# Kernel optimization log

Hardware: AMD Instinct MI355X
Metric: run time of the kernel (lower is better)

The kernel has to match this reference:

```python
import jax, jax.numpy as jnp
import numpy as np

NUM_HEADS = 4


def setup_inputs() -> dict:
    key = jax.random.key(0)
    ks = jax.random.split(key, 12)
    N, E_edges, ND, ED, D, G = 50000, 800000, 128, 64, 256, 128
    h = jax.random.normal(ks[0], (N, ND), dtype=jnp.float32)
    edge_index = jax.random.randint(ks[1], (2, E_edges), 0, N)
    edge_attr = jax.random.normal(ks[2], (E_edges, ED), dtype=jnp.float32)
    batch = jnp.sort(jax.random.randint(ks[3], (N,), 0, G))
    node_w = jax.random.normal(ks[4], (D, ND), dtype=jnp.float32) / np.sqrt(ND)
    node_b = jnp.zeros((D,), dtype=jnp.float32)
    edge_w = jax.random.normal(ks[5], (D, ED), dtype=jnp.float32) / np.sqrt(ED)
    edge_b = jnp.zeros((D,), dtype=jnp.float32)
    query = jax.random.normal(ks[6], (1, D), dtype=jnp.float32)
    in_w = jax.random.normal(ks[7], (3 * D, D), dtype=jnp.float32) / np.sqrt(D)
    in_b = jnp.zeros((3 * D,), dtype=jnp.float32)
    out_w = jax.random.normal(ks[8], (D, D), dtype=jnp.float32) / np.sqrt(D)
    out_b = jnp.zeros((D,), dtype=jnp.float32)
    return {"h": h, "edge_index": edge_index, "edge_attr": edge_attr, "batch": batch,
            "num_graphs": G, "node_w": node_w, "node_b": node_b,
            "edge_w": edge_w, "edge_b": edge_b, "query": query,
            "in_w": in_w, "in_b": in_b, "out_w": out_w, "out_b": out_b}


def reference(h, edge_index, edge_attr, batch, num_graphs,
              node_w, node_b, edge_w, edge_b, query, in_w, in_b, out_w, out_b):
    N = h.shape[0]
    D = query.shape[-1]
    dh = D // NUM_HEADS
    G = num_graphs
    # node projection
    h_proj = h @ node_w.T + node_b  # [N, D]
    # scatter-mean edge features to source nodes
    row = edge_index[0]
    e_proj = edge_attr @ edge_w.T + edge_b  # [E, D]
    e_sum = jax.ops.segment_sum(e_proj, row, num_segments=N)
    cnt = jax.ops.segment_sum(jnp.ones((row.shape[0],), jnp.float32), row, num_segments=N)
    h_proj = h_proj + e_sum / jnp.maximum(cnt, 1.0)[:, None]
    # per-graph single-query multi-head attention (torch MultiheadAttention math)
    wq, wk, wv = in_w[:D], in_w[D:2 * D], in_w[2 * D:]
    bq, bk, bv = in_b[:D], in_b[D:2 * D], in_b[2 * D:]
    q = (query @ wq.T + bq).reshape(NUM_HEADS, dh)            # [H, dh]
    k = (h_proj @ wk.T + bk).reshape(N, NUM_HEADS, dh)        # [N, H, dh]
    v = (h_proj @ wv.T + bv).reshape(N, NUM_HEADS, dh)        # [N, H, dh]
    scores = jnp.einsum('hd,nhd->nh', q, k) / jnp.sqrt(jnp.float32(dh))  # [N, H]
    smax = jax.ops.segment_max(scores, batch, num_segments=G)  # [G, H]
    w = jnp.exp(scores - smax[batch])                          # [N, H]
    denom = jax.ops.segment_sum(w, batch, num_segments=G)      # [G, H]
    p = w / jnp.maximum(denom[batch], 1e-30)                   # [N, H]
    pooled = jax.ops.segment_sum(p[:, :, None] * v, batch, num_segments=G)  # [G, H, dh]
    out = pooled.reshape(G, 1, D) @ out_w.T + out_b            # [G, 1, D]
    return out
```

## Files before the change

### kernel.cpp

```cpp
#include <hip/hip_runtime.h>
#include <hip/hip_bf16.h>
#include <math.h>

#define NDIM 128
#define EDIM 64
#define DDIM 256
#define NSPLIT 4
#define CAP 96
#define SNODES 32

typedef __attribute__((ext_vector_type(8))) short short8;

__device__ inline ushort f2bf(float x) {
    uint32_t u = __float_as_uint(x);
    uint32_t r = (u + 0x7fff + ((u >> 16) & 1)) >> 16;
    return (ushort)r;
}
__device__ inline float bf2f(ushort h) { return __uint_as_float(((uint32_t)h) << 16); }

__global__ __launch_bounds__(256) void k_setup(
    int* __restrict__ zero_p, int n_zero, int ZBLK,
    const float* __restrict__ node_w, const float* __restrict__ edge_w,
    const float* __restrict__ node_b, const float* __restrict__ edge_b,
    const float* __restrict__ query, const float* __restrict__ in_w,
    const float* __restrict__ in_b, float* __restrict__ prep)
{
    const int tid = threadIdx.x;
    int b = blockIdx.x;
    if (b < ZBLK) {
        int i = b * 256 + tid;
        if (i < n_zero) zero_p[i] = 0;
        return;
    }
    __shared__ float q_s[DDIM];
    __shared__ float qv[DDIM];
    __shared__ float qk_s[4 * DDIM];
    __shared__ float sb_s[4];
    q_s[tid] = query[tid];
    __syncthreads();
    float acc = in_b[tid];
    const float* wq = in_w + (size_t)tid * DDIM;
    for (int i = 0; i < DDIM; ++i) acc += q_s[i] * wq[i];
    qv[tid] = acc;
    __syncthreads();
    for (int h = 0; h < 4; ++h) {
        float a = 0.f;
        for (int d = 0; d < 64; ++d)
            a += qv[h * 64 + d] * in_w[(size_t)(DDIM + h * 64 + d) * DDIM + tid];
        qk_s[h * DDIM + tid] = a;
    }
    if (tid < 4) {
        float a = 0.f;
        for (int d = 0; d < 64; ++d) a += qv[tid * 64 + d] * in_b[DDIM + tid * 64 + d];
        sb_s[tid] = a;
    }
    __syncthreads();
    for (int idx = tid; idx < 4 * NDIM; idx += 256) {
        int hh = idx >> 7, k = idx & 127;
        float a = 0.f;
        for (int j = 0; j < DDIM; ++j) a += qk_s[hh * DDIM + j] * node_w[(size_t)j * NDIM + k];
        prep[idx] = a;
    }
    {
        int hh = tid >> 6, k = tid & 63;
        float a = 0.f;
        for (int j = 0; j < DDIM; ++j) a += qk_s[hh * DDIM + j] * edge_w[(size_t)j * EDIM + k];
        prep[4 * NDIM + tid] = a;
    }
    if (tid < 4) {
        float a = 0.f, e = 0.f;
        for (int j = 0; j < DDIM; ++j) {
            a += node_b[j] * qk_s[tid * DDIM + j];
            e += edge_b[j] * qk_s[tid * DDIM + j];
        }
        prep[4 * NDIM + 256 + tid] = a + sb_s[tid];
        prep[4 * NDIM + 260 + tid] = e;
    }
}

__global__ __launch_bounds__(256) void k_scatbin(
    const int* __restrict__ erow, const float* __restrict__ edge_attr,
    int* __restrict__ fill, ushort* __restrict__ ebin, int E)
{
    int gid = blockIdx.x * 256 + threadIdx.x;
    int e = gid >> 3;
    int seg8 = gid & 7;
    if (e >= E) return;
    int r = erow[e];
    int pos = 0;
    if (seg8 == 0) pos = atomicAdd(&fill[r], 1);
    pos = __shfl(pos, 0, 8);
    if (pos >= CAP) return;
    const float* ea = edge_attr + (size_t)e * EDIM + seg8 * 8;
    float4 va = *reinterpret_cast<const float4*>(ea);
    float4 vb = *reinterpret_cast<const float4*>(ea + 4);
    short8 o;
    o[0] = (short)f2bf(va.x); o[1] = (short)f2bf(va.y);
    o[2] = (short)f2bf(va.z); o[3] = (short)f2bf(va.w);
    o[4] = (short)f2bf(vb.x); o[5] = (short)f2bf(vb.y);
    o[6] = (short)f2bf(vb.z); o[7] = (short)f2bf(vb.w);
    *reinterpret_cast<short8*>(
        ebin + ((size_t)r * CAP + pos) * EDIM + seg8 * 8) = o;
}

__global__ __launch_bounds__(256) void k_score(
    const float* __restrict__ h, const ushort* __restrict__ ebin,
    const int* __restrict__ fill, const float* __restrict__ prep,
    ushort* __restrict__ agg_bf, float* __restrict__ scores, int N)
{
    __shared__ float qkn_s[4 * NDIM];
    __shared__ float qke_s[4 * EDIM];
    __shared__ float cst[8];
    const int tid = threadIdx.x;
    for (int i = tid; i < 4 * NDIM; i += 256) qkn_s[i] = prep[i];
    qke_s[tid] = prep[4 * NDIM + tid];
    if (tid < 8) cst[tid] = prep[4 * NDIM + 256 + tid];
    __syncthreads();

    const int node = blockIdx.x * SNODES + (tid >> 3);
    const int seg8 = tid & 7;
    if (node >= N) return;
    const int cnt = fill[node];
    const float inv = 1.f / fmaxf((float)cnt, 1.f);
    const float fl = (cnt > 0) ? 1.f : 0.f;

    float hd[4] = {0.f, 0.f, 0.f, 0.f};
    const float4* hp = reinterpret_cast<const float4*>(h + (size_t)node * NDIM + seg8 * 16);
#pragma unroll
    for (int q = 0; q < 4; ++q) {
        float4 hv = hp[q];
        int base = seg8 * 16 + q * 4;
#pragma unroll
        for (int hh = 0; hh < 4; ++hh) {
            const float* qp = &qkn_s[hh * NDIM + base];
            hd[hh] += hv.x * qp[0] + hv.y * qp[1] + hv.z * qp[2] + hv.w * qp[3];
        }
    }

    float a[8];
#pragma unroll
    for (int i = 0; i < 8; ++i) a[i] = 0.f;
    {
        const ushort* eb = ebin + (size_t)node * CAP * EDIM + seg8 * 8;
        int c = min(cnt, CAP);
        int j = 0;
        for (; j + 3 < c; j += 4) {
            short8 v0 = *reinterpret_cast<const short8*>(eb + (size_t)(j + 0) * EDIM);
            short8 v1 = *reinterpret_cast<const short8*>(eb + (size_t)(j + 1) * EDIM);
            short8 v2 = *reinterpret_cast<const short8*>(eb + (size_t)(j + 2) * EDIM);
            short8 v3 = *reinterpret_cast<const short8*>(eb + (size_t)(j + 3) * EDIM);
#pragma unroll
            for (int i = 0; i < 8; ++i)
                a[i] += (bf2f((ushort)v0[i]) + bf2f((ushort)v1[i]))
                      + (bf2f((ushort)v2[i]) + bf2f((ushort)v3[i]));
        }
        for (; j < c; ++j) {
            short8 v0 = *reinterpret_cast<const short8*>(eb + (size_t)j * EDIM);
#pragma unroll
            for (int i = 0; i < 8; ++i) a[i] += bf2f((ushort)v0[i]);
        }
    }
    {
        short8 o;
#pragma unroll
        for (int i = 0; i < 8; ++i) o[i] = (short)f2bf(a[i]);
        *reinterpret_cast<short8*>(agg_bf + (size_t)node * EDIM + seg8 * 8) = o;
    }
    float ed[4] = {0.f, 0.f, 0.f, 0.f};
#pragma unroll
    for (int i = 0; i < 8; ++i) {
#pragma unroll
        for (int hh = 0; hh < 4; ++hh)
            ed[hh] += a[i] * qke_s[hh * EDIM + seg8 * 8 + i];
    }
    float t[4];
#pragma unroll
    for (int hh = 0; hh < 4; ++hh) t[hh] = hd[hh] + ed[hh] * inv;
#pragma unroll
    for (int off = 1; off < 8; off <<= 1) {
#pragma unroll
        for (int hh = 0; hh < 4; ++hh) t[hh] += __shfl_xor(t[hh], off);
    }
    if (seg8 == 0) {
        float4 sc;
        sc.x = (t[0] + cst[0] + fl * cst[4]) * 0.125f;
        sc.y = (t[1] + cst[1] + fl * cst[5]) * 0.125f;
        sc.z = (t[2] + cst[2] + fl * cst[6]) * 0.125f;
        sc.w = (t[3] + cst[3] + fl * cst[7]) * 0.125f;
        *reinterpret_cast<float4*>(scores + (size_t)node * 4) = sc;
    }
}

__global__ __launch_bounds__(256) void k_pool(
    const float* __restrict__ h, const ushort* __restrict__ agg_bf,
    const float* __restrict__ scores, const int* __restrict__ batch,
    const int* __restrict__ fill,
    float* __restrict__ pm, float* __restrict__ pdn, float* __restrict__ pe,
    float* __restrict__ pv, float* __restrict__ pu, int N)
{
    __shared__ float sc_s[256 * 4];
    __shared__ float cn_s[256];
    __shared__ float red_a[16];
    __shared__ float red_b[16];
    __shared__ float vred[2][4][NDIM];
    __shared__ float ured[4][4][EDIM];

    const int b = blockIdx.x;
    const int g = b >> 2;
    const int part = b & 3;
    const int tid = threadIdx.x;
    const int lane = tid & 63;
    const int wave = tid >> 6;
    const int dv = tid & 127;
    const int g2 = tid >> 7;
    const int du = tid & 63;
    const int g4 = tid >> 6;

    int lo = 0, hi = N;
    while (lo < hi) { int mid = (lo + hi) >> 1; if (batch[mid] < g) lo = mid + 1; else hi = mid; }
    const int s = lo;
    hi = N;
    while (lo < hi) { int mid = (lo + hi) >> 1; if (batch[mid] < g + 1) lo = mid + 1; else hi = mid; }
    const int e = lo;
    const int len = e - s;
    const int cs = s + (len * part) / NSPLIT;
    const int ce = s + (len * (part + 1)) / NSPLIT;

    float m[4], dn[4], spe[4], v[4], uh[4];
#pragma unroll
    for (int hh = 0; hh < 4; ++hh) {
        m[hh] = -INFINITY; dn[hh] = 0.f; spe[hh] = 0.f; v[hh] = 0.f; uh[hh] = 0.f;
    }

    const int hsel = tid & 3;

    for (int c = cs; c < ce; c += 256) {
        int cn = min(256, ce - c);
        __syncthreads();
        if (tid < cn) {
            *reinterpret_cast<float4*>(&sc_s[tid * 4]) =
                *reinterpret_cast<const float4*>(scores + (size_t)(c + tid) * 4);
            cn_s[tid] = (float)fill[c + tid];
        }
        __syncthreads();

        float lm = -INFINITY;
        for (int n = tid >> 2; n < cn; n += 64) lm = fmaxf(lm, sc_s[n * 4 + hsel]);
#pragma unroll
        for (int off = 4; off < 64; off <<= 1) lm = fmaxf(lm, __shfl_xor(lm, off));
        if (lane < 4) red_a[wave * 4 + lane] = lm;
        __syncthreads();

        float nm[4];
#pragma unroll
        for (int hh = 0; hh < 4; ++hh) {
            float cm = fmaxf(fmaxf(red_a[hh], red_a[4 + hh]),
                             fmaxf(red_a[8 + hh], red_a[12 + hh]));
            nm[hh] = fmaxf(m[hh], cm);
            float sc = expf(m[hh] - nm[hh]);
            dn[hh] *= sc; spe[hh] *= sc; v[hh] *= sc; uh[hh] *= sc;
            m[hh] = nm[hh];
        }
        __syncthreads();

        float mh = (hsel == 0) ? nm[0] : (hsel == 1) ? nm[1] : (hsel == 2) ? nm[2] : nm[3];
        float ld = 0.f, le = 0.f;
        for (int idx = tid; idx < cn * 4; idx += 256) {
            float wv = expf(sc_s[idx] - mh);
            sc_s[idx] = wv;
            ld += wv;
            le += wv * ((cn_s[idx >> 2] > 0.5f) ? 1.f : 0.f);
        }
#pragma unroll
        for (int off = 4; off < 64; off <<= 1) {
            ld += __shfl_xor(ld, off);
            le += __shfl_xor(le, off);
        }
        if (lane < 4) { red_a[wave * 4 + lane] = ld; red_b[wave * 4 + lane] = le; }
        __syncthreads();
#pragma unroll
        for (int hh = 0; hh < 4; ++hh) {
            dn[hh]  += red_a[hh] + red_a[4 + hh] + red_a[8 + hh] + red_a[12 + hh];
            spe[hh] += red_b[hh] + red_b[4 + hh] + red_b[8 + hh] + red_b[12 + hh];
        }

        for (int ln = g2; ln < cn; ln += 2) {
            float val = h[(size_t)(c + ln) * NDIM + dv];
            float4 w4 = *reinterpret_cast<const float4*>(&sc_s[ln * 4]);
            v[0] += w4.x * val; v[1] += w4.y * val;
            v[2] += w4.z * val; v[3] += w4.w * val;
        }
        for (int ln = g4; ln < cn; ln += 4) {
            float val = bf2f(agg_bf[(size_t)(c + ln) * EDIM + du]);
            float ci = 1.f / fmaxf(cn_s[ln], 1.f);
            float4 w4 = *reinterpret_cast<const float4*>(&sc_s[ln * 4]);
            uh[0] += w4.x * ci * val; uh[1] += w4.y * ci * val;
            uh[2] += w4.z * ci * val; uh[3] += w4.w * ci * val;
        }
    }

    __syncthreads();
#pragma unroll
    for (int hh = 0; hh < 4; ++hh) {
        vred[g2][hh][dv] = v[hh];
        ured[g4][hh][du] = uh[hh];
    }
    __syncthreads();

    if (tid < 4) { pm[b * 4 + tid] = m[tid]; pdn[b * 4 + tid] = dn[tid]; pe[b * 4 + tid] = spe[tid]; }
    for (int idx = tid; idx < 4 * NDIM; idx += 256) {
        int hh = idx >> 7, k = idx & 127;
        pv[(size_t)(b * 4 + hh) * NDIM + k] = vred[0][hh][k] + vred[1][hh][k];
    }
    {
        int hh = tid >> 6, k = tid & 63;
        pu[(size_t)(b * 4 + hh) * EDIM + k] =
            ured[0][hh][k] + ured[1][hh][k] + ured[2][hh][k] + ured[3][hh][k];
    }
}

__global__ __launch_bounds__(256) void k_out(
    const float* __restrict__ pm, const float* __restrict__ pdn, const float* __restrict__ pe,
    const float* __restrict__ pv, const float* __restrict__ pu,
    const float* __restrict__ node_w, const float* __restrict__ edge_w,
    const float* __restrict__ node_b, const float* __restrict__ edge_b,
    const float* __restrict__ in_w, const float* __restrict__ in_b,
    const float* __restrict__ out_w, const float* __restrict__ out_b,
    float* __restrict__ out)
{
    __shared__ float vm[4][NDIM];
    __shared__ float um[4][EDIM];
    __shared__ float scp_s[NSPLIT][4];
    __shared__ float dnm_s[4];
    __shared__ float spe_s[4];
    __shared__ float has_s;
    __shared__ float hb_s[4 * DDIM];
    __shared__ float po_s[DDIM];

    const int g = blockIdx.x;
    const int tid = threadIdx.x;
    const int b0 = NSPLIT * g;

    if (tid < 4) {
        float Mh = -INFINITY;
#pragma unroll
        for (int p = 0; p < NSPLIT; ++p) Mh = fmaxf(Mh, pm[(b0 + p) * 4 + tid]);
        float d = 0.f, ee = 0.f;
#pragma unroll
        for (int p = 0; p < NSPLIT; ++p) {
            float mp = pm[(b0 + p) * 4 + tid];
            float scp = (mp == -INFINITY) ? 0.f : expf(mp - Mh);
            scp_s[p][tid] = scp;
            d += pdn[(b0 + p) * 4 + tid] * scp;
            ee += pe[(b0 + p) * 4 + tid] * scp;
        }
        dnm_s[tid] = d;
        spe_s[tid] = ee;
        if (tid == 0) has_s = (Mh > -INFINITY) ? 1.f : 0.f;
    }
    __syncthreads();

    for (int idx = tid; idx < 4 * NDIM; idx += 256) {
        int hh = idx >> 7, k = idx & 127;
        float a = 0.f;
#pragma unroll
        for (int p = 0; p < NSPLIT; ++p)
            a += pv[(size_t)((b0 + p) * 4 + hh) * NDIM + k] * scp_s[p][hh];
        vm[hh][k] = a;
    }
    {
        int hh = tid >> 6, k = tid & 63;
        float a = 0.f;
#pragma unroll
        for (int p = 0; p < NSPLIT; ++p)
            a += pu[(size_t)((b0 + p) * 4 + hh) * EDIM + k] * scp_s[p][hh];
        um[hh][k] = a;
    }
    __syncthreads();

    {
        int j = tid;
        float acch[4];
        float nbj = node_b[j], ebj = edge_b[j];
#pragma unroll
        for (int hh = 0; hh < 4; ++hh) acch[hh] = dnm_s[hh] * nbj + spe_s[hh] * ebj;
        const float4* nwr = reinterpret_cast<const float4*>(node_w + (size_t)j * NDIM);
        for (int q = 0; q < NDIM / 4; ++q) {
            float4 w4 = nwr[q];
#pragma unroll
            for (int hh = 0; hh < 4; ++hh) {
                const float* vp = &vm[hh][q * 4];
                acch[hh] += w4.x * vp[0] + w4.y * vp[1] + w4.z * vp[2] + w4.w * vp[3];
            }
        }
        const float4* ewr = reinterpret_cast<const float4*>(edge_w + (size_t)j * EDIM);
        for (int q = 0; q < EDIM / 4; ++q) {
            float4 w4 = ewr[q];
#pragma unroll
            for (int hh = 0; hh < 4; ++hh) {
                const float* up = &um[hh][q * 4];
                acch[hh] += w4.x * up[0] + w4.y * up[1] + w4.z * up[2] + w4.w * up[3];
            }
        }
#pragma unroll
        for (int hh = 0; hh < 4; ++hh)
            hb_s[hh * DDIM + j] = acch[hh] / fmaxf(dnm_s[hh], 1e-30f);
    }
    __syncthreads();

    const int jh = tid >> 6;
    const float* wv_row = in_w + (size_t)(2 * DDIM + tid) * DDIM;
    const float* hbr = &hb_s[jh * DDIM];
    float p = 0.f;
    for (int i = 0; i < DDIM; i += 4) {
        float4 a = *reinterpret_cast<const float4*>(hbr + i);
        float4 bb = *reinterpret_cast<const float4*>(wv_row + i);
        p += a.x * bb.x + a.y * bb.y + a.z * bb.z + a.w * bb.w;
    }
    p = (p + in_b[2 * DDIM + tid]) * has_s;
    po_s[tid] = p;
    __syncthreads();

    const float* ow_row = out_w + (size_t)tid * DDIM;
    float o = out_b[tid];
    for (int i = 0; i < DDIM; i += 4) {
        float4 a = *reinterpret_cast<const float4*>(&po_s[i]);
        float4 bb = *reinterpret_cast<const float4*>(ow_row + i);
        o += a.x * bb.x + a.y * bb.y + a.z * bb.z + a.w * bb.w;
    }
    out[(size_t)g * DDIM + tid] = o;
}

extern "C" void kernel_launch(void* const* d_in, const int* in_sizes, int n_in,
                              void* d_out, int out_size, void* d_ws, size_t ws_size,
                              hipStream_t stream) {
    const float* h         = (const float*)d_in[0];
    const int*   edge_idx  = (const int*)d_in[1];
    const float* edge_attr = (const float*)d_in[2];
    const int*   batch     = (const int*)d_in[3];
    const float* node_w    = (const float*)d_in[5];
    const float* node_b    = (const float*)d_in[6];
    const float* edge_w    = (const float*)d_in[7];
    const float* edge_b    = (const float*)d_in[8];
    const float* query     = (const float*)d_in[9];
    const float* in_w      = (const float*)d_in[10];
    const float* in_b      = (const float*)d_in[11];
    const float* out_w     = (const float*)d_in[12];
    const float* out_b     = (const float*)d_in[13];
    float* out = (float*)d_out;

    const int N = in_sizes[0] / NDIM;
    const int E = in_sizes[2] / EDIM;
    const int G = out_size / DDIM;

    char* ws = (char*)d_ws;
    size_t off = 0;
    auto alloc = [&](size_t bytes) { void* p = ws + off; off += (bytes + 255) & ~(size_t)255; return p; };

    int*    fill    = (int*)alloc((size_t)N * 4);
    float*  scores  = (float*)alloc((size_t)N * 4 * 4);
    ushort* agg_bf  = (ushort*)alloc((size_t)N * EDIM * 2);
    float*  prep    = (float*)alloc(776 * 4);
    float*  pm      = (float*)alloc((size_t)NSPLIT * G * 4 * 4);
    float*  pdn     = (float*)alloc((size_t)NSPLIT * G * 4 * 4);
    float*  pe      = (float*)alloc((size_t)NSPLIT * G * 4 * 4);
    float*  pv      = (float*)alloc((size_t)NSPLIT * G * 4 * NDIM * 4);
    float*  pu      = (float*)alloc((size_t)NSPLIT * G * 4 * EDIM * 4);
    ushort* ebin    = (ushort*)alloc((size_t)N * CAP * EDIM * 2);

    const int ZBLK = (N + 255) / 256;
    k_setup<<<ZBLK + 1, 256, 0, stream>>>(
        fill, N, ZBLK, node_w, edge_w, node_b, edge_b, query, in_w, in_b, prep);

    k_scatbin<<<((E * 8) + 255) / 256, 256, 0, stream>>>(
        edge_idx, edge_attr, fill, ebin, E);

    k_score<<<(N + SNODES - 1) / SNODES, 256, 0, stream>>>(
        h, ebin, fill, prep, agg_bf, scores, N);

    k_pool<<<NSPLIT * G, 256, 0, stream>>>(
        h, agg_bf, scores, batch, fill, pm, pdn, pe, pv, pu, N);

    k_out<<<G, 256, 0, stream>>>(
        pm, pdn, pe, pv, pu, node_w, edge_w, node_b, edge_b,
        in_w, in_b, out_w, out_b, out);
}
```

Baseline: 196.9 us.

## Replace fixed-capacity edge bins with exact CSR layout via histogram and prefix scan

Edges were previously binned per source node into fixed slots of capacity 96, and edges beyond that capacity were dropped. The change builds a histogram of source rows, runs a two-pass prefix scan to get per-node offsets, and scatters bf16 edge features into a compact CSR buffer sized by the edge count. This shrinks the bin buffer and makes the per-node edge reads contiguous. It also removes the silent truncation, so results stay correct for any degree. In exchange it adds three small kernel launches and a second pass over the edge indices. k_scan3 sums the block totals with one 64-lane wavefront, so it assumes N is at most 64*1024.

```diff
diff --git a/kernel.cpp b/kernel.cpp
--- a/kernel.cpp
+++ b/kernel.cpp
@@ -6,7 +6,6 @@
 #define EDIM 64
 #define DDIM 256
 #define NSPLIT 4
-#define CAP 96
 #define SNODES 32
 
 typedef __attribute__((ext_vector_type(8))) short short8;
@@ -78,9 +77,73 @@
     }
 }
 
+__global__ __launch_bounds__(256) void k_hist(
+    const int* __restrict__ erow, int* __restrict__ cnt, int E)
+{
+    int e = blockIdx.x * 256 + threadIdx.x;
+    if (e < E) atomicAdd(&cnt[erow[e]], 1);
+}
+
+__global__ __launch_bounds__(256) void k_scan1(
+    const int* __restrict__ cnt, int* __restrict__ blocksum, int N)
+{
+    int tid = threadIdx.x;
+    int i0 = blockIdx.x * 1024 + tid * 4;
+    int s = 0;
+#pragma unroll
+    for (int k = 0; k < 4; ++k) { int i = i0 + k; if (i < N) s += cnt[i]; }
+#pragma unroll
+    for (int off = 1; off < 64; off <<= 1) s += __shfl_xor(s, off);
+    __shared__ int ws4[4];
+    if ((tid & 63) == 0) ws4[tid >> 6] = s;
+    __syncthreads();
+    if (tid == 0) blocksum[blockIdx.x] = ws4[0] + ws4[1] + ws4[2] + ws4[3];
+}
+
+__global__ __launch_bounds__(256) void k_scan3(
+    const int* __restrict__ cnt, const int* __restrict__ blocksum,
+    int* __restrict__ base, int N)
+{
+    const int tid = threadIdx.x;
+    const int lane = tid & 63;
+    const int wv = tid >> 6;
+    const int b = blockIdx.x;
+    const int i0 = b * 1024 + tid * 4;
+
+    int v[4];
+#pragma unroll
+    for (int k = 0; k < 4; ++k) { int i = i0 + k; v[k] = (i < N) ? cnt[i] : 0; }
+    int tsum = v[0] + v[1] + v[2] + v[3];
+
+    int incl = tsum;
+#pragma unroll
+    for (int off = 1; off < 64; off <<= 1) {
+        int x = __shfl_up(incl, off);
+        if (lane >= off) incl += x;
+    }
+    __shared__ int wsum[4];
+    if (lane == 63) wsum[wv] = incl;
+    __syncthreads();
+    int wpre = 0;
+    for (int w = 0; w < wv; ++w) wpre += wsum[w];
+
+    int bb = (lane < b) ? blocksum[lane] : 0;
+#pragma unroll
+    for (int off = 1; off < 64; off <<= 1) bb += __shfl_xor(bb, off);
+
+    int excl = bb + wpre + incl - tsum;
+#pragma unroll
+    for (int k = 0; k < 4; ++k) {
+        int i = i0 + k;
+        if (i < N) base[i] = excl;
+        excl += v[k];
+    }
+}
+
 __global__ __launch_bounds__(256) void k_scatbin(
     const int* __restrict__ erow, const float* __restrict__ edge_attr,
-    int* __restrict__ fill, ushort* __restrict__ ebin, int E)
+    const int* __restrict__ base, int* __restrict__ fill,
+    ushort* __restrict__ ebin, int E)
 {
     int gid = blockIdx.x * 256 + threadIdx.x;
     int e = gid >> 3;
@@ -88,9 +151,8 @@
     if (e >= E) return;
     int r = erow[e];
     int pos = 0;
-    if (seg8 == 0) pos = atomicAdd(&fill[r], 1);
+    if (seg8 == 0) pos = base[r] + atomicAdd(&fill[r], 1);
     pos = __shfl(pos, 0, 8);
-    if (pos >= CAP) return;
     const float* ea = edge_attr + (size_t)e * EDIM + seg8 * 8;
     float4 va = *reinterpret_cast<const float4*>(ea);
     float4 vb = *reinterpret_cast<const float4*>(ea + 4);
@@ -99,13 +161,13 @@
     o[2] = (short)f2bf(va.z); o[3] = (short)f2bf(va.w);
     o[4] = (short)f2bf(vb.x); o[5] = (short)f2bf(vb.y);
     o[6] = (short)f2bf(vb.z); o[7] = (short)f2bf(vb.w);
-    *reinterpret_cast<short8*>(
-        ebin + ((size_t)r * CAP + pos) * EDIM + seg8 * 8) = o;
+    *reinterpret_cast<short8*>(ebin + (size_t)pos * EDIM + seg8 * 8) = o;
 }
 
 __global__ __launch_bounds__(256) void k_score(
     const float* __restrict__ h, const ushort* __restrict__ ebin,
-    const int* __restrict__ fill, const float* __restrict__ prep,
+    const int* __restrict__ base, const int* __restrict__ cnt,
+    const float* __restrict__ prep,
     ushort* __restrict__ agg_bf, float* __restrict__ scores, int N)
 {
     __shared__ float qkn_s[4 * NDIM];
@@ -120,19 +182,20 @@
     const int node = blockIdx.x * SNODES + (tid >> 3);
     const int seg8 = tid & 7;
     if (node >= N) return;
-    const int cnt = fill[node];
-    const float inv = 1.f / fmaxf((float)cnt, 1.f);
-    const float fl = (cnt > 0) ? 1.f : 0.f;
+    const int c = cnt[node];
+    const int bs = base[node];
+    const float inv = 1.f / fmaxf((float)c, 1.f);
+    const float fl = (c > 0) ? 1.f : 0.f;
 
     float hd[4] = {0.f, 0.f, 0.f, 0.f};
     const float4* hp = reinterpret_cast<const float4*>(h + (size_t)node * NDIM + seg8 * 16);
 #pragma unroll
     for (int q = 0; q < 4; ++q) {
         float4 hv = hp[q];
-        int base = seg8 * 16 + q * 4;
+        int bq = seg8 * 16 + q * 4;
 #pragma unroll
         for (int hh = 0; hh < 4; ++hh) {
-            const float* qp = &qkn_s[hh * NDIM + base];
+            const float* qp = &qkn_s[hh * NDIM + bq];
             hd[hh] += hv.x * qp[0] + hv.y * qp[1] + hv.z * qp[2] + hv.w * qp[3];
         }
     }
@@ -141,8 +204,7 @@
 #pragma unroll
     for (int i = 0; i < 8; ++i) a[i] = 0.f;
     {
-        const ushort* eb = ebin + (size_t)node * CAP * EDIM + seg8 * 8;
-        int c = min(cnt, CAP);
+        const ushort* eb = ebin + (size_t)bs * EDIM + seg8 * 8;
         int j = 0;
         for (; j + 3 < c; j += 4) {
             short8 v0 = *reinterpret_cast<const short8*>(eb + (size_t)(j + 0) * EDIM);
@@ -194,7 +256,7 @@
 __global__ __launch_bounds__(256) void k_pool(
     const float* __restrict__ h, const ushort* __restrict__ agg_bf,
     const float* __restrict__ scores, const int* __restrict__ batch,
-    const int* __restrict__ fill,
+    const int* __restrict__ cnt,
     float* __restrict__ pm, float* __restrict__ pdn, float* __restrict__ pe,
     float* __restrict__ pv, float* __restrict__ pu, int N)
 {
@@ -240,7 +302,7 @@
         if (tid < cn) {
             *reinterpret_cast<float4*>(&sc_s[tid * 4]) =
                 *reinterpret_cast<const float4*>(scores + (size_t)(c + tid) * 4);
-            cn_s[tid] = (float)fill[c + tid];
+            cn_s[tid] = (float)cnt[c + tid];
         }
         __syncthreads();
 
@@ -452,12 +514,16 @@
     const int N = in_sizes[0] / NDIM;
     const int E = in_sizes[2] / EDIM;
     const int G = out_size / DDIM;
+    const int nblk1 = (N + 1023) / 1024;
 
     char* ws = (char*)d_ws;
     size_t off = 0;
     auto alloc = [&](size_t bytes) { void* p = ws + off; off += (bytes + 255) & ~(size_t)255; return p; };
 
-    int*    fill    = (int*)alloc((size_t)N * 4);
+    int*    cnt     = (int*)alloc((size_t)N * 4 * 2);
+    int*    fill    = cnt + N;
+    int*    base    = (int*)alloc((size_t)N * 4);
+    int*    blocksum= (int*)alloc((size_t)nblk1 * 4);
     float*  scores  = (float*)alloc((size_t)N * 4 * 4);
     ushort* agg_bf  = (ushort*)alloc((size_t)N * EDIM * 2);
     float*  prep    = (float*)alloc(776 * 4);
@@ -466,20 +532,24 @@
     float*  pe      = (float*)alloc((size_t)NSPLIT * G * 4 * 4);
     float*  pv      = (float*)alloc((size_t)NSPLIT * G * 4 * NDIM * 4);
     float*  pu      = (float*)alloc((size_t)NSPLIT * G * 4 * EDIM * 4);
-    ushort* ebin    = (ushort*)alloc((size_t)N * CAP * EDIM * 2);
-
-    const int ZBLK = (N + 255) / 256;
+    ushort* ebin    = (ushort*)alloc((size_t)E * EDIM * 2);
+
+    const int ZBLK = (2 * N + 255) / 256;
     k_setup<<<ZBLK + 1, 256, 0, stream>>>(
-        fill, N, ZBLK, node_w, edge_w, node_b, edge_b, query, in_w, in_b, prep);
+        cnt, 2 * N, ZBLK, node_w, edge_w, node_b, edge_b, query, in_w, in_b, prep);
+
+    k_hist<<<(E + 255) / 256, 256, 0, stream>>>(edge_idx, cnt, E);
+    k_scan1<<<nblk1, 256, 0, stream>>>(cnt, blocksum, N);
+    k_scan3<<<nblk1, 256, 0, stream>>>(cnt, blocksum, base, N);
 
     k_scatbin<<<((E * 8) + 255) / 256, 256, 0, stream>>>(
-        edge_idx, edge_attr, fill, ebin, E);
+        edge_idx, edge_attr, base, fill, ebin, E);
 
     k_score<<<(N + SNODES - 1) / SNODES, 256, 0, stream>>>(
-        h, ebin, fill, prep, agg_bf, scores, N);
+        h, ebin, base, cnt, prep, agg_bf, scores, N);
 
     k_pool<<<NSPLIT * G, 256, 0, stream>>>(
-        h, agg_bf, scores, batch, fill, pm, pdn, pe, pv, pu, N);
+        h, agg_bf, scores, batch, cnt, pm, pdn, pe, pv, pu, N);
 
     k_out<<<G, 256, 0, stream>>>(
         pm, pdn, pe, pv, pu, node_w, edge_w, node_b, edge_b,
```

Measured after the change: 230.1 us. +16.9%, slower.

## Fuse per-node score computation into the per-graph pooling kernel

Applied to the files above, without the earlier changes.

Moves the per-node score and edge-aggregate computation into the pooling kernel, keeping scores and aggregated edge features in shared memory instead of global buffers. This removes one kernel launch and the global write/read of scores and the bf16 aggregates. In exchange the bandwidth-heavy edge-bin reduction now runs in only NSPLIT*G blocks with large shared memory use, which reduces parallelism and occupancy.

```diff
diff --git a/kernel.cpp b/kernel.cpp
--- a/kernel.cpp
+++ b/kernel.cpp
@@ -7,7 +7,7 @@
 #define DDIM 256
 #define NSPLIT 4
 #define CAP 96
-#define SNODES 32
+#define AGS 72
 
 typedef __attribute__((ext_vector_type(8))) short short8;
 
@@ -103,103 +103,19 @@
         ebin + ((size_t)r * CAP + pos) * EDIM + seg8 * 8) = o;
 }
 
-__global__ __launch_bounds__(256) void k_score(
+__global__ __launch_bounds__(256) void k_poolscore(
     const float* __restrict__ h, const ushort* __restrict__ ebin,
     const int* __restrict__ fill, const float* __restrict__ prep,
-    ushort* __restrict__ agg_bf, float* __restrict__ scores, int N)
+    const int* __restrict__ batch,
+    float* __restrict__ pm, float* __restrict__ pdn, float* __restrict__ pe,
+    float* __restrict__ pv, float* __restrict__ pu, int N)
 {
+    __shared__ ushort agg_s[256 * AGS];
+    __shared__ float sc_s[256 * 4];
+    __shared__ float cn_s[256];
     __shared__ float qkn_s[4 * NDIM];
     __shared__ float qke_s[4 * EDIM];
     __shared__ float cst[8];
-    const int tid = threadIdx.x;
-    for (int i = tid; i < 4 * NDIM; i += 256) qkn_s[i] = prep[i];
-    qke_s[tid] = prep[4 * NDIM + tid];
-    if (tid < 8) cst[tid] = prep[4 * NDIM + 256 + tid];
-    __syncthreads();
-
-    const int node = blockIdx.x * SNODES + (tid >> 3);
-    const int seg8 = tid & 7;
-    if (node >= N) return;
-    const int cnt = fill[node];
-    const float inv = 1.f / fmaxf((float)cnt, 1.f);
-    const float fl = (cnt > 0) ? 1.f : 0.f;
-
-    float hd[4] = {0.f, 0.f, 0.f, 0.f};
-    const float4* hp = reinterpret_cast<const float4*>(h + (size_t)node * NDIM + seg8 * 16);
-#pragma unroll
-    for (int q = 0; q < 4; ++q) {
-        float4 hv = hp[q];
-        int base = seg8 * 16 + q * 4;
-#pragma unroll
-        for (int hh = 0; hh < 4; ++hh) {
-            const float* qp = &qkn_s[hh * NDIM + base];
-            hd[hh] += hv.x * qp[0] + hv.y * qp[1] + hv.z * qp[2] + hv.w * qp[3];
-        }
-    }
-
-    float a[8];
-#pragma unroll
-    for (int i = 0; i < 8; ++i) a[i] = 0.f;
-    {
-        const ushort* eb = ebin + (size_t)node * CAP * EDIM + seg8 * 8;
-        int c = min(cnt, CAP);
-        int j = 0;
-        for (; j + 3 < c; j += 4) {
-            short8 v0 = *reinterpret_cast<const short8*>(eb + (size_t)(j + 0) * EDIM);
-            short8 v1 = *reinterpret_cast<const short8*>(eb + (size_t)(j + 1) * EDIM);
-            short8 v2 = *reinterpret_cast<const short8*>(eb + (size_t)(j + 2) * EDIM);
-            short8 v3 = *reinterpret_cast<const short8*>(eb + (size_t)(j + 3) * EDIM);
-#pragma unroll
-            for (int i = 0; i < 8; ++i)
-                a[i] += (bf2f((ushort)v0[i]) + bf2f((ushort)v1[i]))
-                      + (bf2f((ushort)v2[i]) + bf2f((ushort)v3[i]));
-        }
-        for (; j < c; ++j) {
-            short8 v0 = *reinterpret_cast<const short8*>(eb + (size_t)j * EDIM);
-#pragma unroll
-            for (int i = 0; i < 8; ++i) a[i] += bf2f((ushort)v0[i]);
-        }
-    }
-    {
-        short8 o;
-#pragma unroll
-        for (int i = 0; i < 8; ++i) o[i] = (short)f2bf(a[i]);
-        *reinterpret_cast<short8*>(agg_bf + (size_t)node * EDIM + seg8 * 8) = o;
-    }
-    float ed[4] = {0.f, 0.f, 0.f, 0.f};
-#pragma unroll
-    for (int i = 0; i < 8; ++i) {
-#pragma unroll
-        for (int hh = 0; hh < 4; ++hh)
-            ed[hh] += a[i] * qke_s[hh * EDIM + seg8 * 8 + i];
-    }
-    float t[4];
-#pragma unroll
-    for (int hh = 0; hh < 4; ++hh) t[hh] = hd[hh] + ed[hh] * inv;
-#pragma unroll
-    for (int off = 1; off < 8; off <<= 1) {
-#pragma unroll
-        for (int hh = 0; hh < 4; ++hh) t[hh] += __shfl_xor(t[hh], off);
-    }
-    if (seg8 == 0) {
-        float4 sc;
-        sc.x = (t[0] + cst[0] + fl * cst[4]) * 0.125f;
-        sc.y = (t[1] + cst[1] + fl * cst[5]) * 0.125f;
-        sc.z = (t[2] + cst[2] + fl * cst[6]) * 0.125f;
-        sc.w = (t[3] + cst[3] + fl * cst[7]) * 0.125f;
-        *reinterpret_cast<float4*>(scores + (size_t)node * 4) = sc;
-    }
-}
-
-__global__ __launch_bounds__(256) void k_pool(
-    const float* __restrict__ h, const ushort* __restrict__ agg_bf,
-    const float* __restrict__ scores, const int* __restrict__ batch,
-    const int* __restrict__ fill,
-    float* __restrict__ pm, float* __restrict__ pdn, float* __restrict__ pe,
-    float* __restrict__ pv, float* __restrict__ pu, int N)
-{
-    __shared__ float sc_s[256 * 4];
-    __shared__ float cn_s[256];
     __shared__ float red_a[16];
     __shared__ float red_b[16];
     __shared__ float vred[2][4][NDIM];
@@ -215,6 +131,11 @@
     const int g2 = tid >> 7;
     const int du = tid & 63;
     const int g4 = tid >> 6;
+    const int seg8 = tid & 7;
+
+    for (int i = tid; i < 4 * NDIM; i += 256) qkn_s[i] = prep[i];
+    qke_s[tid] = prep[4 * NDIM + tid];
+    if (tid < 8) cst[tid] = prep[4 * NDIM + 256 + tid];
 
     int lo = 0, hi = N;
     while (lo < hi) { int mid = (lo + hi) >> 1; if (batch[mid] < g) lo = mid + 1; else hi = mid; }
@@ -237,10 +158,84 @@
     for (int c = cs; c < ce; c += 256) {
         int cn = min(256, ce - c);
         __syncthreads();
-        if (tid < cn) {
-            *reinterpret_cast<float4*>(&sc_s[tid * 4]) =
-                *reinterpret_cast<const float4*>(scores + (size_t)(c + tid) * 4);
-            cn_s[tid] = (float)fill[c + tid];
+        if (tid < cn) cn_s[tid] = (float)fill[c + tid];
+        __syncthreads();
+
+        for (int pass = 0; pass < 8; ++pass) {
+            int node_l = pass * 32 + (tid >> 3);
+            if (node_l < cn) {
+                int n = c + node_l;
+                float cntf = cn_s[node_l];
+                int ci = min((int)cntf, CAP);
+                float inv = 1.f / fmaxf(cntf, 1.f);
+                float fl = (cntf > 0.5f) ? 1.f : 0.f;
+
+                float hd[4] = {0.f, 0.f, 0.f, 0.f};
+                const float4* hp = reinterpret_cast<const float4*>(
+                    h + (size_t)n * NDIM + seg8 * 16);
+#pragma unroll
+                for (int q = 0; q < 4; ++q) {
+                    float4 hv = hp[q];
+                    int bq = seg8 * 16 + q * 4;
+#pragma unroll
+                    for (int hh = 0; hh < 4; ++hh) {
+                        const float* qp = &qkn_s[hh * NDIM + bq];
+                        hd[hh] += hv.x * qp[0] + hv.y * qp[1] + hv.z * qp[2] + hv.w * qp[3];
+                    }
+                }
+
+                float a[8];
+#pragma unroll
+                for (int i = 0; i < 8; ++i) a[i] = 0.f;
+                {
+                    const ushort* eb = ebin + ((size_t)n * CAP) * EDIM + seg8 * 8;
+                    int j = 0;
+                    for (; j + 3 < ci; j += 4) {
+                        short8 v0 = *reinterpret_cast<const short8*>(eb + (size_t)(j + 0) * EDIM);
+                        short8 v1 = *reinterpret_cast<const short8*>(eb + (size_t)(j + 1) * EDIM);
+                        short8 v2 = *reinterpret_cast<const short8*>(eb + (size_t)(j + 2) * EDIM);
+                        short8 v3 = *reinterpret_cast<const short8*>(eb + (size_t)(j + 3) * EDIM);
+#pragma unroll
+                        for (int i = 0; i < 8; ++i)
+                            a[i] += (bf2f((ushort)v0[i]) + bf2f((ushort)v1[i]))
+                                  + (bf2f((ushort)v2[i]) + bf2f((ushort)v3[i]));
+                    }
+                    for (; j < ci; ++j) {
+                        short8 v0 = *reinterpret_cast<const short8*>(eb + (size_t)j * EDIM);
+#pragma unroll
+                        for (int i = 0; i < 8; ++i) a[i] += bf2f((ushort)v0[i]);
+                    }
+                }
+                {
+                    short8 o;
+#pragma unroll
+                    for (int i = 0; i < 8; ++i) o[i] = (short)f2bf(a[i]);
+                    *reinterpret_cast<short8*>(&agg_s[node_l * AGS + seg8 * 8]) = o;
+                }
+                float ed[4] = {0.f, 0.f, 0.f, 0.f};
+#pragma unroll
+                for (int i = 0; i < 8; ++i) {
+#pragma unroll
+                    for (int hh = 0; hh < 4; ++hh)
+                        ed[hh] += a[i] * qke_s[hh * EDIM + seg8 * 8 + i];
+                }
+                float t[4];
+#pragma unroll
+                for (int hh = 0; hh < 4; ++hh) t[hh] = hd[hh] + ed[hh] * inv;
+#pragma unroll
+                for (int off = 1; off < 8; off <<= 1) {
+#pragma unroll
+                    for (int hh = 0; hh < 4; ++hh) t[hh] += __shfl_xor(t[hh], off);
+                }
+                if (seg8 == 0) {
+                    float4 sc;
+                    sc.x = (t[0] + cst[0] + fl * cst[4]) * 0.125f;
+                    sc.y = (t[1] + cst[1] + fl * cst[5]) * 0.125f;
+                    sc.z = (t[2] + cst[2] + fl * cst[6]) * 0.125f;
+                    sc.w = (t[3] + cst[3] + fl * cst[7]) * 0.125f;
+                    *reinterpret_cast<float4*>(&sc_s[node_l * 4]) = sc;
+                }
+            }
         }
         __syncthreads();
 
@@ -291,7 +286,7 @@
             v[2] += w4.z * val; v[3] += w4.w * val;
         }
         for (int ln = g4; ln < cn; ln += 4) {
-            float val = bf2f(agg_bf[(size_t)(c + ln) * EDIM + du]);
+            float val = bf2f(agg_s[ln * AGS + du]);
             float ci = 1.f / fmaxf(cn_s[ln], 1.f);
             float4 w4 = *reinterpret_cast<const float4*>(&sc_s[ln * 4]);
             uh[0] += w4.x * ci * val; uh[1] += w4.y * ci * val;
@@ -458,8 +453,6 @@
     auto alloc = [&](size_t bytes) { void* p = ws + off; off += (bytes + 255) & ~(size_t)255; return p; };
 
     int*    fill    = (int*)alloc((size_t)N * 4);
-    float*  scores  = (float*)alloc((size_t)N * 4 * 4);
-    ushort* agg_bf  = (ushort*)alloc((size_t)N * EDIM * 2);
     float*  prep    = (float*)alloc(776 * 4);
     float*  pm      = (float*)alloc((size_t)NSPLIT * G * 4 * 4);
     float*  pdn     = (float*)alloc((size_t)NSPLIT * G * 4 * 4);
@@ -475,11 +468,8 @@
     k_scatbin<<<((E * 8) + 255) / 256, 256, 0, stream>>>(
         edge_idx, edge_attr, fill, ebin, E);
 
-    k_score<<<(N + SNODES - 1) / SNODES, 256, 0, stream>>>(
-        h, ebin, fill, prep, agg_bf, scores, N);
-
-    k_pool<<<NSPLIT * G, 256, 0, stream>>>(
-        h, agg_bf, scores, batch, fill, pm, pdn, pe, pv, pu, N);
+    k_poolscore<<<NSPLIT * G, 256, 0, stream>>>(
+        h, ebin, fill, prep, batch, pm, pdn, pe, pv, pu, N);
 
     k_out<<<G, 256, 0, stream>>>(
         pm, pdn, pe, pv, pu, node_w, edge_w, node_b, edge_b,
```

New measurement: 186.3 us. 1.06x faster.
